# Kernel tuning notes

Hardware: AMD Instinct MI355X
Metric: run time of the kernel (lower is better)

The kernel has to match this reference:

```python
import jax, jax.numpy as jnp
import numpy as np

HID, INTER, DK = 768, 1536, 128
NEG_INF = 1.0e12
LOG512 = float(np.log(512.0))


def setup_inputs() -> dict:
    key = jax.random.key(0)
    k1, k2, k3 = jax.random.split(key, 3)
    B, S = 4, 2048
    hidden_states = jax.random.normal(k1, (B, S, HID), dtype=jnp.float32)
    attention_mask = jnp.ones((B, S), dtype=jnp.int32)
    # i_dense: hidden -> 2*INTER + DK (no bias); o_dense: INTER -> hidden (no bias)
    Wi = jax.random.normal(k2, (HID, 2 * INTER + DK), dtype=jnp.float32) * (HID ** -0.5)
    Wo = jax.random.normal(k3, (INTER, HID), dtype=jnp.float32) * (INTER ** -0.5)
    q_gamma = jnp.ones((DK,), dtype=jnp.float32)  # ScaleOffset scale, offset=False
    k_gamma = jnp.ones((DK,), dtype=jnp.float32)
    return {"hidden_states": hidden_states, "Wi": Wi, "Wo": Wo,
            "q_gamma": q_gamma, "k_gamma": k_gamma,
            "attention_mask": attention_mask}


def reference(hidden_states, Wi, Wo, q_gamma, k_gamma, attention_mask):
    # i_dense + swish, then split into u, v, qk
    x = jax.nn.silu(jnp.einsum('bsh,ho->bso', hidden_states, Wi))
    u = x[..., :INTER]
    v = x[..., INTER:2 * INTER]
    qk = x[..., 2 * INTER:]
    q = qk * q_gamma
    k = qk * k_gamma
    # single-head attention scores
    a = jnp.einsum('bmd,bnd->bmn', q, k) / (DK ** 0.5)
    mask = attention_mask[:, None, :]  # [B,1,N]
    a = jnp.where(mask == 0, -NEG_INF, a)
    l = jnp.sum(attention_mask, axis=-1, keepdims=True)[:, :, None].astype(a.dtype)  # [B,1,1]
    # softmax_plus: softmax(a * log(l) / log(512))
    A = jax.nn.softmax(a * jnp.log(l) / LOG512, axis=-1)
    # dropout inactive in eval mode
    o = jnp.einsum('bmi,ih->bmh', u * jnp.einsum('bmn,bnd->bmd', A, v), Wo)
    return o
```

## Files before the change

### kernel.cpp

```cpp
#include <hip/hip_runtime.h>
#include <hip/hip_bf16.h>
#include <math.h>

#define BATCH 4
#define SEQ   2048
#define HID   768
#define INTER 1536
#define DK    128
#define NTOT  3200
#define NTOTP 3328
#define MROWS 8192
#define LN512 6.2383246250395075f

typedef _Float16 half8   __attribute__((ext_vector_type(8)));
typedef _Float16 half4   __attribute__((ext_vector_type(4)));
typedef float    floatx4 __attribute__((ext_vector_type(4)));
typedef float    floatx16 __attribute__((ext_vector_type(16)));

typedef const __attribute__((address_space(1))) unsigned int* gas1_t;
typedef __attribute__((address_space(3))) unsigned int* las3_t;

static __device__ __forceinline__ void load16(const _Float16* g, _Float16* l) {
    __builtin_amdgcn_global_load_lds((gas1_t)g, (las3_t)l, 16, 0, 0);
}
#define WAIT_VM(N)    asm volatile("s_waitcnt vmcnt(" #N ")" ::: "memory")
#define WAIT_LGKM0()  asm volatile("s_waitcnt lgkmcnt(0)" ::: "memory")
#define BARRIER_RAW() asm volatile("s_barrier" ::: "memory")

__global__ void cast_h_kernel(const float* __restrict__ in, _Float16* __restrict__ out, int n) {
    int i = (blockIdx.x * blockDim.x + threadIdx.x) * 8;
    if (i < n) {
        float4 a = *reinterpret_cast<const float4*>(in + i);
        float4 b = *reinterpret_cast<const float4*>(in + i + 4);
        half8 h = {(_Float16)a.x, (_Float16)a.y, (_Float16)a.z, (_Float16)a.w,
                   (_Float16)b.x, (_Float16)b.y, (_Float16)b.z, (_Float16)b.w};
        *reinterpret_cast<half8*>(out + i) = h;
    }
}

__global__ void trans_wi_kernel(const float* __restrict__ Wi, _Float16* __restrict__ WiT) {
    __shared__ _Float16 tile[32][33];
    const int c0 = blockIdx.x * 32, r0 = blockIdx.y * 32;
    const int tx = threadIdx.x, ty = threadIdx.y;
#pragma unroll
    for (int j = 0; j < 32; j += 8)
        tile[tx][ty + j] = (c0 + tx < NTOT)
            ? (_Float16)Wi[(size_t)(r0 + ty + j) * NTOT + c0 + tx]
            : (_Float16)0.0f;
    __syncthreads();
#pragma unroll
    for (int j = 0; j < 32; j += 8)
        WiT[(size_t)(c0 + ty + j) * HID + r0 + tx] = tile[ty + j][tx];
}

__global__ void trans_wo_kernel(const float* __restrict__ Wo, _Float16* __restrict__ WoT) {
    __shared__ _Float16 tile[32][33];
    const int c0 = blockIdx.x * 32, r0 = blockIdx.y * 32;
    const int tx = threadIdx.x, ty = threadIdx.y;
#pragma unroll
    for (int j = 0; j < 32; j += 8)
        tile[tx][ty + j] = (_Float16)Wo[(size_t)(r0 + ty + j) * HID + c0 + tx];
    __syncthreads();
#pragma unroll
    for (int j = 0; j < 32; j += 8)
        WoT[(size_t)(c0 + ty + j) * INTER + r0 + tx] = tile[ty + j][tx];
}

__global__ void mask_scales_kernel(const int* __restrict__ mask, float* __restrict__ scales) {
    __shared__ int sh[256];
    int b = blockIdx.x;
    int s = 0;
    for (int i = threadIdx.x; i < SEQ; i += 256) s += mask[b * SEQ + i];
    sh[threadIdx.x] = s;
    __syncthreads();
    for (int off = 128; off > 0; off >>= 1) {
        if (threadIdx.x < off) sh[threadIdx.x] += sh[threadIdx.x + off];
        __syncthreads();
    }
    if (threadIdx.x == 0) scales[b] = logf((float)sh[0]) / LN512;
}

struct TileCtx {
    int tid, wave, lane, quad, l16, l31, half, wm, wn, c0, c1;
};
static __device__ __forceinline__ TileCtx make_ctx() {
    TileCtx t;
    t.tid = threadIdx.x;
    t.wave = t.tid >> 6; t.lane = t.tid & 63;
    t.quad = t.lane >> 4; t.l16 = t.lane & 15;
    t.l31 = t.lane & 31;  t.half = t.lane >> 5;
    t.wm = (t.wave & 1) * 64;
    t.wn = (t.wave >> 1) * 64;
    t.c0 = t.tid;
    t.c1 = t.tid + 256;
    return t;
}

static __device__ __forceinline__ void gemm_mainloop_3s32(
    const TileCtx& t,
    const _Float16* __restrict__ Ag, int lda,
    const _Float16* __restrict__ Bg, int ldb,
    int K, _Float16* smem, floatx16 acc[2][2])
{
    const int r0i = t.c0 >> 2, s0 = (((r0i >> 1) ^ (r0i >> 3)) & 3);
    const int r1i = t.c1 >> 2, s1 = (((r1i >> 1) ^ (r1i >> 3)) & 3);
    const int ak0 = ((t.c0 & 3) ^ s0) * 8;
    const int ak1 = ((t.c1 & 3) ^ s1) * 8;
    const _Float16* a0 = Ag + (size_t)r0i * lda + ak0;
    const _Float16* a1 = Ag + (size_t)r1i * lda + ak1;
    const _Float16* b0 = Bg + (size_t)r0i * ldb + ak0;
    const _Float16* b1 = Bg + (size_t)r1i * ldb + ak1;
    _Float16* Asl = smem + t.c0 * 8;
    _Float16* Bsl = smem + 12288 + t.c0 * 8;
    const int nIter = K >> 5;

    const int fsw = ((t.l31 >> 1) ^ (t.l31 >> 3)) & 3;

    load16(a0, Asl);        load16(a1, Asl + 2048);
    load16(b0, Bsl);        load16(b1, Bsl + 2048);
    if (nIter > 1) {
        load16(a0 + 32, Asl + 4096); load16(a1 + 32, Asl + 6144);
        load16(b0 + 32, Bsl + 4096); load16(b1 + 32, Bsl + 6144);
    }

    int sc = 0, sp = 2;
    for (int k = 0; k < nIter; ++k) {
        if (k + 1 < nIter) { WAIT_VM(4); } else { WAIT_VM(0); }
        BARRIER_RAW();
        if (k + 2 < nIter) {
            const int off = sp * 4096;
            const int k0 = (k + 2) << 5;
            load16(a0 + k0, Asl + off); load16(a1 + k0, Asl + off + 2048);
            load16(b0 + k0, Bsl + off); load16(b1 + k0, Bsl + off + 2048);
        }
        const _Float16* Ab = smem + sc * 4096;
        const _Float16* Bb = smem + 12288 + sc * 4096;
        half8 af[2][2], bf[2][2];
#pragma unroll
        for (int mt = 0; mt < 2; ++mt)
#pragma unroll
            for (int h = 0; h < 2; ++h)
                af[mt][h] = *reinterpret_cast<const half8*>(
                    Ab + (t.wm + mt * 32 + t.l31) * 32 + (((h * 2 + t.half) ^ fsw) * 8));
#pragma unroll
        for (int nt = 0; nt < 2; ++nt)
#pragma unroll
            for (int h = 0; h < 2; ++h)
                bf[nt][h] = *reinterpret_cast<const half8*>(
                    Bb + (t.wn + nt * 32 + t.l31) * 32 + (((h * 2 + t.half) ^ fsw) * 8));
#pragma unroll
        for (int h = 0; h < 2; ++h)
#pragma unroll
            for (int mt = 0; mt < 2; ++mt)
#pragma unroll
                for (int nt = 0; nt < 2; ++nt)
                    acc[mt][nt] = __builtin_amdgcn_mfma_f32_32x32x16_f16(af[mt][h], bf[nt][h], acc[mt][nt], 0, 0, 0);
        WAIT_LGKM0();
        sc = (sc == 2) ? 0 : sc + 1;
        sp = (sp == 2) ? 0 : sp + 1;
    }
}

__global__ __launch_bounds__(512, 2) void gemm1_kernel(
    const _Float16* __restrict__ Hb, const _Float16* __restrict__ WiT,
    const float* __restrict__ qg, const float* __restrict__ kg,
    _Float16* __restrict__ u, _Float16* __restrict__ vT,
    _Float16* __restrict__ q, _Float16* __restrict__ k)
{
    __shared__ _Float16 smem[65536];
    const int tid = threadIdx.x;
    const int lane = tid & 63, wave = tid >> 6;
    const int quad = lane >> 4, l16 = lane & 15;
    const int wm = wave >> 2, wn = wave & 3;

    const int f = blockIdx.x;
    const int xcd = f & 7, i = f >> 3;
    const int m0 = (xcd * 4 + (i & 3)) * 256;
    const int ntile = i >> 2;
    const int n0 = ntile * 256;

    const _Float16* Ag = Hb  + (size_t)m0 * HID;
    const _Float16* Bg = WiT + (size_t)n0 * HID;

    const int rA = tid >> 2;
    const int csw = ((tid & 3) ^ ((rA >> 1) & 3)) * 8;
    const _Float16* pa0 = Ag + (size_t)rA * HID + csw;
    const _Float16* pa1 = pa0 + (size_t)128 * HID;
    const _Float16* pb0 = Bg + (size_t)rA * HID + csw;
    const _Float16* pb1 = pb0 + (size_t)128 * HID;

    const int sw8 = (l16 >> 1) & 3;
    const int qs  = (quad ^ sw8) * 8;
    const int aoff = (wm * 128 + l16) * 32 + qs;
    const int boff = 8192 + (wn * 64 + l16) * 32 + qs;

    floatx4 acc[8][4] = {};

    const int nKt = HID / 32;

#pragma unroll
    for (int pt = 0; pt < 3; ++pt) {
        _Float16* ld = smem + pt * 16384 + tid * 8;
        const int ko = pt * 32;
        load16(pa0 + ko, ld);
        load16(pa1 + ko, ld + 4096);
        load16(pb0 + ko, ld + 8192);
        load16(pb1 + ko, ld + 12288);
    }
    WAIT_VM(8);
    BARRIER_RAW();

    for (int t = 0; t < nKt; ++t) {
        const _Float16* sl = smem + (t & 3) * 16384;
        if (t + 3 < nKt) {
            _Float16* ld = smem + ((t + 3) & 3) * 16384 + tid * 8;
            const int ko = (t + 3) * 32;
            load16(pa0 + ko, ld);        load16(pa1 + ko, ld + 4096);
            load16(pb0 + ko, ld + 8192); load16(pb1 + ko, ld + 12288);
        }
        half8 af[8], bf[4];
#pragma unroll
        for (int mt = 0; mt < 8; ++mt)
            af[mt] = *reinterpret_cast<const half8*>(sl + aoff + mt * 512);
#pragma unroll
        for (int nt = 0; nt < 4; ++nt)
            bf[nt] = *reinterpret_cast<const half8*>(sl + boff + nt * 512);
        __builtin_amdgcn_s_setprio(1);
#pragma unroll
        for (int mt = 0; mt < 8; ++mt)
#pragma unroll
            for (int nt = 0; nt < 4; ++nt)
                acc[mt][nt] = __builtin_amdgcn_mfma_f32_16x16x32_f16(af[mt], bf[nt], acc[mt][nt], 0, 0, 0);
        __builtin_amdgcn_s_setprio(0);
        if (t <= nKt - 4)      { WAIT_VM(8); }
        else if (t == nKt - 3) { WAIT_VM(4); }
        else if (t == nKt - 2) { WAIT_VM(0); }
        BARRIER_RAW();
    }
    __syncthreads();

    if (ntile < 6) {
#pragma unroll
        for (int mt = 0; mt < 8; ++mt) {
#pragma unroll
            for (int nt = 0; nt < 4; ++nt) {
                const int col = n0 + wn * 64 + nt * 16 + l16;
#pragma unroll
                for (int i2 = 0; i2 < 4; ++i2) {
                    const int row = m0 + wm * 128 + mt * 16 + quad * 4 + i2;
                    float x = acc[mt][nt][i2];
                    float y = x / (1.0f + __expf(-x));
                    u[(size_t)row * INTER + col] = (_Float16)y;
                }
            }
        }
    } else if (ntile < 12) {
        const int bb = m0 >> 11, sloc = m0 & (SEQ - 1), cI = n0 - INTER;
#pragma unroll
        for (int mt = 0; mt < 8; ++mt) {
#pragma unroll
            for (int nt = 0; nt < 4; ++nt) {
                const int cl  = wn * 64 + nt * 16 + l16;
                const int rl0 = wm * 128 + mt * 16 + quad * 4;
                half4 pk;
#pragma unroll
                for (int i2 = 0; i2 < 4; ++i2) {
                    float x = acc[mt][nt][i2];
                    pk[i2] = (_Float16)(x / (1.0f + __expf(-x)));
                }
                *reinterpret_cast<half4*>(smem + cl * 256 + (rl0 ^ ((cl & 31) << 3))) = pk;
            }
        }
        __syncthreads();
#pragma unroll
        for (int p = 0; p < 16; ++p) {
            const int chunk = p * 512 + tid;
            const int cl = chunk >> 5, scn = chunk & 31;
            half8 v = *reinterpret_cast<const half8*>(smem + cl * 256 + ((scn ^ (cl & 31)) << 3));
            *reinterpret_cast<half8*>(vT + ((size_t)bb * INTER + cI + cl) * SEQ + sloc + scn * 8) = v;
        }
    } else {
        if (wn < 2) {
#pragma unroll
            for (int mt = 0; mt < 8; ++mt) {
#pragma unroll
                for (int nt = 0; nt < 4; ++nt) {
                    const int cq = wn * 64 + nt * 16 + l16;
                    const float qgv = qg[cq], kgv = kg[cq];
#pragma unroll
                    for (int i2 = 0; i2 < 4; ++i2) {
                        const int row = m0 + wm * 128 + mt * 16 + quad * 4 + i2;
                        float x = acc[mt][nt][i2];
                        float y = x / (1.0f + __expf(-x));
                        q[(size_t)row * DK + cq] = (_Float16)(y * qgv);
                        k[(size_t)row * DK + cq] = (_Float16)(y * kgv);
                    }
                }
            }
        }
    }
}

__global__ __launch_bounds__(256) void scores_kernel(
    const _Float16* __restrict__ q, const _Float16* __restrict__ k,
    const int* __restrict__ mask, const float* __restrict__ scales,
    _Float16* __restrict__ P)
{
    const int f = blockIdx.x;
    const int xcd = f & 7, i = f >> 3;
    const int b = xcd >> 1;
    const int m0 = ((xcd & 1) * 64 + i) * 16;
    const int tid = threadIdx.x;
    const int wave = tid >> 6, lane = tid & 63, quad = lane >> 4, l16 = lane & 15;
    const float scale = scales[b];

    half8 aq[4];
    const _Float16* qrow = q + (b * SEQ + m0 + l16) * DK + quad * 8;
#pragma unroll
    for (int kk = 0; kk < 4; ++kk) aq[kk] = *reinterpret_cast<const half8*>(qrow + kk * 32);

    floatx4 sc[32];
#pragma unroll
    for (int nt = 0; nt < 32; ++nt) {
        int n0 = nt * 64 + wave * 16;
        const _Float16* krow = k + (b * SEQ + n0 + l16) * DK + quad * 8;
        floatx4 acc = {};
#pragma unroll
        for (int kk = 0; kk < 4; ++kk) {
            half8 bq = *reinterpret_cast<const half8*>(krow + kk * 32);
            acc = __builtin_amdgcn_mfma_f32_16x16x32_f16(aq[kk], bq, acc, 0, 0, 0);
        }
        sc[nt] = acc;
    }

    const float rs = 0.08838834764831845f * scale;
    const float mval = -1e12f * scale;
    float rmax[4] = {-3.4e38f, -3.4e38f, -3.4e38f, -3.4e38f};
#pragma unroll
    for (int nt = 0; nt < 32; ++nt) {
        int ncol = nt * 64 + wave * 16 + l16;
        bool mok = mask[b * SEQ + ncol] != 0;
#pragma unroll
        for (int i2 = 0; i2 < 4; ++i2) {
            float s = mok ? sc[nt][i2] * rs : mval;
            sc[nt][i2] = s;
            rmax[i2] = fmaxf(rmax[i2], s);
        }
    }
#pragma unroll
    for (int i2 = 0; i2 < 4; ++i2) {
#pragma unroll
        for (int off = 1; off < 16; off <<= 1)
            rmax[i2] = fmaxf(rmax[i2], __shfl_xor(rmax[i2], off, 64));
    }
    __shared__ float redmax[4][16];
    __shared__ float redsum[4][16];
    if (l16 == 0) {
#pragma unroll
        for (int i2 = 0; i2 < 4; ++i2) redmax[wave][quad * 4 + i2] = rmax[i2];
    }
    __syncthreads();
#pragma unroll
    for (int i2 = 0; i2 < 4; ++i2) {
        int r = quad * 4 + i2;
        rmax[i2] = fmaxf(fmaxf(redmax[0][r], redmax[1][r]), fmaxf(redmax[2][r], redmax[3][r]));
    }
    float rsum[4] = {0.f, 0.f, 0.f, 0.f};
#pragma unroll
    for (int nt = 0; nt < 32; ++nt) {
#pragma unroll
        for (int i2 = 0; i2 < 4; ++i2) {
            float e = __expf(sc[nt][i2] - rmax[i2]);
            sc[nt][i2] = e;
            rsum[i2] += e;
        }
    }
#pragma unroll
    for (int i2 = 0; i2 < 4; ++i2) {
#pragma unroll
        for (int off = 1; off < 16; off <<= 1) rsum[i2] += __shfl_xor(rsum[i2], off, 64);
    }
    if (l16 == 0) {
#pragma unroll
        for (int i2 = 0; i2 < 4; ++i2) redsum[wave][quad * 4 + i2] = rsum[i2];
    }
    __syncthreads();
#pragma unroll
    for (int i2 = 0; i2 < 4; ++i2) {
        int r = quad * 4 + i2;
        float tot = redsum[0][r] + redsum[1][r] + redsum[2][r] + redsum[3][r];
        float inv = 1.0f / tot;
        int row = m0 + r;
        _Float16* Prow = P + ((size_t)b * SEQ + row) * SEQ;
#pragma unroll
        for (int nt = 0; nt < 32; ++nt) {
            int ncol = nt * 64 + wave * 16 + l16;
            Prow[ncol] = (_Float16)(sc[nt][i2] * inv);
        }
    }
}

__global__ __launch_bounds__(256) void pv_kernel(
    const _Float16* __restrict__ P, const _Float16* __restrict__ vT,
    _Float16* __restrict__ u)
{
    __shared__ _Float16 smem[24576];
    TileCtx t = make_ctx();
    const int f = blockIdx.x;
    const int xcd = f & 7, i = f >> 3;
    const int b = i / 24, j = i % 24;
    const int m0 = (xcd * 2 + (j & 1)) * 128;
    const int n0 = (j >> 1) * 128;
    const _Float16* Pb  = P  + (size_t)b * SEQ * SEQ;
    const _Float16* vTb = vT + (size_t)b * INTER * SEQ;

    floatx16 acc[2][2] = {};
    gemm_mainloop_3s32(t, Pb + (size_t)m0 * SEQ, SEQ, vTb + (size_t)n0 * SEQ, SEQ, SEQ, smem, acc);

#pragma unroll
    for (int mt = 0; mt < 2; ++mt) {
#pragma unroll
        for (int nt = 0; nt < 2; ++nt) {
            int col = n0 + t.wn + nt * 32 + t.l31;
#pragma unroll
            for (int reg = 0; reg < 16; ++reg) {
                int row = m0 + t.wm + mt * 32 + (reg & 3) + 8 * (reg >> 2) + 4 * t.half;
                size_t gidx = ((size_t)(b * SEQ + row)) * INTER + col;
                float uv = (float)u[gidx];
                u[gidx] = (_Float16)(acc[mt][nt][reg] * uv);
            }
        }
    }
}

__global__ __launch_bounds__(256) void gemm2_kernel(
    const _Float16* __restrict__ tin, const _Float16* __restrict__ WoT,
    float* __restrict__ out)
{
    __shared__ _Float16 smem[24576];
    TileCtx t = make_ctx();
    const int f = blockIdx.x;
    const int xcd = f & 7, i = f >> 3;
    const int m0 = ((xcd << 3) | (i & 7)) * 128;
    const int n0 = (i >> 3) * 128;

    floatx16 acc[2][2] = {};
    gemm_mainloop_3s32(t, tin + (size_t)m0 * INTER, INTER, WoT + (size_t)n0 * INTER, INTER, INTER, smem, acc);

#pragma unroll
    for (int mt = 0; mt < 2; ++mt) {
#pragma unroll
        for (int nt = 0; nt < 2; ++nt) {
            int col = n0 + t.wn + nt * 32 + t.l31;
#pragma unroll
            for (int reg = 0; reg < 16; ++reg) {
                int row = m0 + t.wm + mt * 32 + (reg & 3) + 8 * (reg >> 2) + 4 * t.half;
                out[(size_t)row * HID + col] = acc[mt][nt][reg];
            }
        }
    }
}

extern "C" void kernel_launch(void* const* d_in, const int* in_sizes, int n_in,
                              void* d_out, int out_size, void* d_ws, size_t ws_size,
                              hipStream_t stream) {
    const float* H    = (const float*)d_in[0];
    const float* Wi   = (const float*)d_in[1];
    const float* Wo   = (const float*)d_in[2];
    const float* qg   = (const float*)d_in[3];
    const float* kg   = (const float*)d_in[4];
    const int*   mask = (const int*)d_in[5];
    float* out = (float*)d_out;

    char* base = (char*)d_ws;
    size_t off = 0;
    auto alloc = [&](size_t bytes) { void* p = base + off; off = (off + bytes + 255) & ~(size_t)255; return p; };
    _Float16* Hb   = (_Float16*)alloc((size_t)MROWS * HID * 2);
    _Float16* WiT  = (_Float16*)alloc((size_t)NTOTP * HID * 2);
    _Float16* WoT  = (_Float16*)alloc((size_t)HID * INTER * 2);
    _Float16* u    = (_Float16*)alloc((size_t)MROWS * INTER * 2);
    _Float16* vT   = (_Float16*)alloc((size_t)BATCH * INTER * SEQ * 2);
    _Float16* q    = (_Float16*)alloc((size_t)MROWS * DK * 2);
    _Float16* k    = (_Float16*)alloc((size_t)MROWS * DK * 2);
    _Float16* P    = (_Float16*)alloc((size_t)BATCH * SEQ * SEQ * 2);
    float*    scales = (float*)alloc(4 * sizeof(float));

    {
        int n = MROWS * HID;
        cast_h_kernel<<<n / 8 / 256, 256, 0, stream>>>(H, Hb, n);
        trans_wi_kernel<<<dim3(NTOTP / 32, HID / 32), dim3(32, 8), 0, stream>>>(Wi, WiT);
        trans_wo_kernel<<<dim3(HID / 32, INTER / 32), dim3(32, 8), 0, stream>>>(Wo, WoT);
        mask_scales_kernel<<<BATCH, 256, 0, stream>>>(mask, scales);
    }
    gemm1_kernel<<<416, 512, 0, stream>>>(Hb, WiT, qg, kg, u, vT, q, k);
    scores_kernel<<<512, 256, 0, stream>>>(q, k, mask, scales, P);
    pv_kernel<<<768, 256, 0, stream>>>(P, vT, u);
    gemm2_kernel<<<384, 256, 0, stream>>>(u, WoT, out);
}
```

Baseline: 304.5 us.

## Rework shared GEMM mainloop with 4-stage column-major LDS pipeline and priority hints

Replaces the 3-stage swizzled LDS mainloop used by the PV and output GEMMs with a 4-buffer pipeline that prefetches three K-tiles ahead, stores tiles in a k-chunk-major layout instead of an XOR swizzle, and moves the barrier to the end of each iteration. It also raises wave priority around the MFMA block. The aim is to hide more global-load latency and drop the per-iteration LDS wait. The cost is more shared memory per block (32K halves), which may lower occupancy, and the new layout may bring LDS bank conflicts back.

```diff
diff --git a/kernel.cpp b/kernel.cpp
--- a/kernel.cpp
+++ b/kernel.cpp
@@ -24,7 +24,6 @@
     __builtin_amdgcn_global_load_lds((gas1_t)g, (las3_t)l, 16, 0, 0);
 }
 #define WAIT_VM(N)    asm volatile("s_waitcnt vmcnt(" #N ")" ::: "memory")
-#define WAIT_LGKM0()  asm volatile("s_waitcnt lgkmcnt(0)" ::: "memory")
 #define BARRIER_RAW() asm volatile("s_barrier" ::: "memory")
 
 __global__ void cast_h_kernel(const float* __restrict__ in, _Float16* __restrict__ out, int n) {
@@ -81,7 +80,7 @@
 }
 
 struct TileCtx {
-    int tid, wave, lane, quad, l16, l31, half, wm, wn, c0, c1;
+    int tid, wave, lane, quad, l16, l31, half, wm, wn;
 };
 static __device__ __forceinline__ TileCtx make_ctx() {
     TileCtx t;
@@ -91,63 +90,61 @@
     t.l31 = t.lane & 31;  t.half = t.lane >> 5;
     t.wm = (t.wave & 1) * 64;
     t.wn = (t.wave >> 1) * 64;
-    t.c0 = t.tid;
-    t.c1 = t.tid + 256;
     return t;
 }
 
-static __device__ __forceinline__ void gemm_mainloop_3s32(
+static __device__ __forceinline__ void gemm_mainloop_cm32(
     const TileCtx& t,
     const _Float16* __restrict__ Ag, int lda,
     const _Float16* __restrict__ Bg, int ldb,
     int K, _Float16* smem, floatx16 acc[2][2])
 {
-    const int r0i = t.c0 >> 2, s0 = (((r0i >> 1) ^ (r0i >> 3)) & 3);
-    const int r1i = t.c1 >> 2, s1 = (((r1i >> 1) ^ (r1i >> 3)) & 3);
-    const int ak0 = ((t.c0 & 3) ^ s0) * 8;
-    const int ak1 = ((t.c1 & 3) ^ s1) * 8;
-    const _Float16* a0 = Ag + (size_t)r0i * lda + ak0;
-    const _Float16* a1 = Ag + (size_t)r1i * lda + ak1;
-    const _Float16* b0 = Bg + (size_t)r0i * ldb + ak0;
-    const _Float16* b1 = Bg + (size_t)r1i * ldb + ak1;
-    _Float16* Asl = smem + t.c0 * 8;
-    _Float16* Bsl = smem + 12288 + t.c0 * 8;
-    const int nIter = K >> 5;
-
-    const int fsw = ((t.l31 >> 1) ^ (t.l31 >> 3)) & 3;
-
-    load16(a0, Asl);        load16(a1, Asl + 2048);
-    load16(b0, Bsl);        load16(b1, Bsl + 2048);
-    if (nIter > 1) {
-        load16(a0 + 32, Asl + 4096); load16(a1 + 32, Asl + 6144);
-        load16(b0 + 32, Bsl + 4096); load16(b1 + 32, Bsl + 6144);
-    }
-
-    int sc = 0, sp = 2;
-    for (int k = 0; k < nIter; ++k) {
-        if (k + 1 < nIter) { WAIT_VM(4); } else { WAIT_VM(0); }
-        BARRIER_RAW();
-        if (k + 2 < nIter) {
-            const int off = sp * 4096;
-            const int k0 = (k + 2) << 5;
-            load16(a0 + k0, Asl + off); load16(a1 + k0, Asl + off + 2048);
-            load16(b0 + k0, Bsl + off); load16(b1 + k0, Bsl + off + 2048);
-        }
-        const _Float16* Ab = smem + sc * 4096;
-        const _Float16* Bb = smem + 12288 + sc * 4096;
+    const int rst = t.tid & 127;
+    const int c08 = (t.tid >> 7) * 8;
+    const _Float16* pa = Ag + (size_t)rst * lda + c08;
+    const _Float16* pb = Bg + (size_t)rst * ldb + c08;
+    const int nKt = K >> 5;
+
+    const int arow = t.wm + t.l31;
+    const int brow = t.wn + t.l31;
+
+#pragma unroll
+    for (int pt = 0; pt < 3; ++pt) {
+        _Float16* ld = smem + pt * 8192 + t.tid * 8;
+        const int ko = pt * 32;
+        load16(pa + ko,      ld);
+        load16(pa + ko + 16, ld + 2048);
+        load16(pb + ko,      ld + 4096);
+        load16(pb + ko + 16, ld + 6144);
+    }
+    WAIT_VM(8);
+    BARRIER_RAW();
+
+    for (int k = 0; k < nKt; ++k) {
+        const _Float16* Ab = smem + (k & 3) * 8192;
+        const _Float16* Bb = Ab + 4096;
+        if (k + 3 < nKt) {
+            _Float16* ld = smem + ((k + 3) & 3) * 8192 + t.tid * 8;
+            const int ko = (k + 3) * 32;
+            load16(pa + ko,      ld);
+            load16(pa + ko + 16, ld + 2048);
+            load16(pb + ko,      ld + 4096);
+            load16(pb + ko + 16, ld + 6144);
+        }
         half8 af[2][2], bf[2][2];
 #pragma unroll
         for (int mt = 0; mt < 2; ++mt)
 #pragma unroll
             for (int h = 0; h < 2; ++h)
                 af[mt][h] = *reinterpret_cast<const half8*>(
-                    Ab + (t.wm + mt * 32 + t.l31) * 32 + (((h * 2 + t.half) ^ fsw) * 8));
+                    Ab + (h * 2 + t.half) * 1024 + (arow + mt * 32) * 8);
 #pragma unroll
         for (int nt = 0; nt < 2; ++nt)
 #pragma unroll
             for (int h = 0; h < 2; ++h)
                 bf[nt][h] = *reinterpret_cast<const half8*>(
-                    Bb + (t.wn + nt * 32 + t.l31) * 32 + (((h * 2 + t.half) ^ fsw) * 8));
+                    Bb + (h * 2 + t.half) * 1024 + (brow + nt * 32) * 8);
+        __builtin_amdgcn_s_setprio(1);
 #pragma unroll
         for (int h = 0; h < 2; ++h)
 #pragma unroll
@@ -155,9 +152,11 @@
 #pragma unroll
                 for (int nt = 0; nt < 2; ++nt)
                     acc[mt][nt] = __builtin_amdgcn_mfma_f32_32x32x16_f16(af[mt][h], bf[nt][h], acc[mt][nt], 0, 0, 0);
-        WAIT_LGKM0();
-        sc = (sc == 2) ? 0 : sc + 1;
-        sp = (sp == 2) ? 0 : sp + 1;
+        __builtin_amdgcn_s_setprio(0);
+        if (k <= nKt - 4)      { WAIT_VM(8); }
+        else if (k == nKt - 3) { WAIT_VM(4); }
+        else if (k == nKt - 2) { WAIT_VM(0); }
+        BARRIER_RAW();
     }
 }
 
@@ -404,7 +403,7 @@
     const _Float16* __restrict__ P, const _Float16* __restrict__ vT,
     _Float16* __restrict__ u)
 {
-    __shared__ _Float16 smem[24576];
+    __shared__ _Float16 smem[32768];
     TileCtx t = make_ctx();
     const int f = blockIdx.x;
     const int xcd = f & 7, i = f >> 3;
@@ -415,7 +414,7 @@
     const _Float16* vTb = vT + (size_t)b * INTER * SEQ;
 
     floatx16 acc[2][2] = {};
-    gemm_mainloop_3s32(t, Pb + (size_t)m0 * SEQ, SEQ, vTb + (size_t)n0 * SEQ, SEQ, SEQ, smem, acc);
+    gemm_mainloop_cm32(t, Pb + (size_t)m0 * SEQ, SEQ, vTb + (size_t)n0 * SEQ, SEQ, SEQ, smem, acc);
 
 #pragma unroll
     for (int mt = 0; mt < 2; ++mt) {
@@ -437,7 +436,7 @@
     const _Float16* __restrict__ tin, const _Float16* __restrict__ WoT,
     float* __restrict__ out)
 {
-    __shared__ _Float16 smem[24576];
+    __shared__ _Float16 smem[32768];
     TileCtx t = make_ctx();
     const int f = blockIdx.x;
     const int xcd = f & 7, i = f >> 3;
@@ -445,7 +444,7 @@
     const int n0 = (i >> 3) * 128;
 
     floatx16 acc[2][2] = {};
-    gemm_mainloop_3s32(t, tin + (size_t)m0 * INTER, INTER, WoT + (size_t)n0 * INTER, INTER, INTER, smem, acc);
+    gemm_mainloop_cm32(t, tin + (size_t)m0 * INTER, INTER, WoT + (size_t)n0 * INTER, INTER, INTER, smem, acc);
 
 #pragma unroll
     for (int mt = 0; mt < 2; ++mt) {
```

Result: slower. 358.6 us (+17.8%).

## Merge prep kernels into one launch and stage P stores through LDS

Applied to the files above, without the earlier changes.

The four preprocessing kernels (cast H, transpose Wi, transpose Wo, mask scales) become one kernel that dispatches on block index, removing three launches and the gaps between them. The scores kernel now writes the normalized probabilities into a padded shared-memory tile and then copies whole rows to global memory with 16-byte vector stores, instead of scattered 2-byte stores. This adds about 64KB of LDS per block, which may lower occupancy in the scores kernel.

```diff
diff --git a/kernel.cpp b/kernel.cpp
--- a/kernel.cpp
+++ b/kernel.cpp
@@ -27,57 +27,58 @@
 #define WAIT_LGKM0()  asm volatile("s_waitcnt lgkmcnt(0)" ::: "memory")
 #define BARRIER_RAW() asm volatile("s_barrier" ::: "memory")
 
-__global__ void cast_h_kernel(const float* __restrict__ in, _Float16* __restrict__ out, int n) {
-    int i = (blockIdx.x * blockDim.x + threadIdx.x) * 8;
-    if (i < n) {
-        float4 a = *reinterpret_cast<const float4*>(in + i);
-        float4 b = *reinterpret_cast<const float4*>(in + i + 4);
+__global__ __launch_bounds__(256) void prep_kernel(
+    const float* __restrict__ H, _Float16* __restrict__ Hb,
+    const float* __restrict__ Wi, _Float16* __restrict__ WiT,
+    const float* __restrict__ Wo, _Float16* __restrict__ WoT,
+    const int* __restrict__ mask, float* __restrict__ scales)
+{
+    __shared__ _Float16 tile[32][33];
+    __shared__ int sh[256];
+    const int bid = blockIdx.x, tid = threadIdx.x;
+    if (bid < 3072) {
+        const int i = (bid * 256 + tid) * 8;
+        float4 a = *reinterpret_cast<const float4*>(H + i);
+        float4 b = *reinterpret_cast<const float4*>(H + i + 4);
         half8 h = {(_Float16)a.x, (_Float16)a.y, (_Float16)a.z, (_Float16)a.w,
                    (_Float16)b.x, (_Float16)b.y, (_Float16)b.z, (_Float16)b.w};
-        *reinterpret_cast<half8*>(out + i) = h;
-    }
-}
-
-__global__ void trans_wi_kernel(const float* __restrict__ Wi, _Float16* __restrict__ WiT) {
-    __shared__ _Float16 tile[32][33];
-    const int c0 = blockIdx.x * 32, r0 = blockIdx.y * 32;
-    const int tx = threadIdx.x, ty = threadIdx.y;
-#pragma unroll
-    for (int j = 0; j < 32; j += 8)
-        tile[tx][ty + j] = (c0 + tx < NTOT)
-            ? (_Float16)Wi[(size_t)(r0 + ty + j) * NTOT + c0 + tx]
-            : (_Float16)0.0f;
-    __syncthreads();
-#pragma unroll
-    for (int j = 0; j < 32; j += 8)
-        WiT[(size_t)(c0 + ty + j) * HID + r0 + tx] = tile[ty + j][tx];
-}
-
-__global__ void trans_wo_kernel(const float* __restrict__ Wo, _Float16* __restrict__ WoT) {
-    __shared__ _Float16 tile[32][33];
-    const int c0 = blockIdx.x * 32, r0 = blockIdx.y * 32;
-    const int tx = threadIdx.x, ty = threadIdx.y;
-#pragma unroll
-    for (int j = 0; j < 32; j += 8)
-        tile[tx][ty + j] = (_Float16)Wo[(size_t)(r0 + ty + j) * HID + c0 + tx];
-    __syncthreads();
-#pragma unroll
-    for (int j = 0; j < 32; j += 8)
-        WoT[(size_t)(c0 + ty + j) * INTER + r0 + tx] = tile[ty + j][tx];
-}
-
-__global__ void mask_scales_kernel(const int* __restrict__ mask, float* __restrict__ scales) {
-    __shared__ int sh[256];
-    int b = blockIdx.x;
-    int s = 0;
-    for (int i = threadIdx.x; i < SEQ; i += 256) s += mask[b * SEQ + i];
-    sh[threadIdx.x] = s;
-    __syncthreads();
-    for (int off = 128; off > 0; off >>= 1) {
-        if (threadIdx.x < off) sh[threadIdx.x] += sh[threadIdx.x + off];
+        *reinterpret_cast<half8*>(Hb + i) = h;
+    } else if (bid < 3072 + 2496) {
+        const int l = bid - 3072;
+        const int c0 = (l % 104) * 32, r0 = (l / 104) * 32;
+        const int tx = tid & 31, ty = tid >> 5;
+#pragma unroll
+        for (int j = 0; j < 32; j += 8)
+            tile[tx][ty + j] = (c0 + tx < NTOT)
+                ? (_Float16)Wi[(size_t)(r0 + ty + j) * NTOT + c0 + tx]
+                : (_Float16)0.0f;
         __syncthreads();
-    }
-    if (threadIdx.x == 0) scales[b] = logf((float)sh[0]) / LN512;
+#pragma unroll
+        for (int j = 0; j < 32; j += 8)
+            WiT[(size_t)(c0 + ty + j) * HID + r0 + tx] = tile[ty + j][tx];
+    } else if (bid < 3072 + 2496 + 1152) {
+        const int l = bid - (3072 + 2496);
+        const int c0 = (l % 24) * 32, r0 = (l / 24) * 32;
+        const int tx = tid & 31, ty = tid >> 5;
+#pragma unroll
+        for (int j = 0; j < 32; j += 8)
+            tile[tx][ty + j] = (_Float16)Wo[(size_t)(r0 + ty + j) * HID + c0 + tx];
+        __syncthreads();
+#pragma unroll
+        for (int j = 0; j < 32; j += 8)
+            WoT[(size_t)(c0 + ty + j) * INTER + r0 + tx] = tile[ty + j][tx];
+    } else {
+        const int b = bid - (3072 + 2496 + 1152);
+        int s = 0;
+        for (int i = tid; i < SEQ; i += 256) s += mask[b * SEQ + i];
+        sh[tid] = s;
+        __syncthreads();
+        for (int off = 128; off > 0; off >>= 1) {
+            if (tid < off) sh[tid] += sh[tid + off];
+            __syncthreads();
+        }
+        if (tid == 0) scales[b] = logf((float)sh[0]) / LN512;
+    }
 }
 
 struct TileCtx {
@@ -306,6 +307,9 @@
     const int* __restrict__ mask, const float* __restrict__ scales,
     _Float16* __restrict__ P)
 {
+    __shared__ _Float16 ps[16 * 2056];
+    __shared__ float redmax[4][16];
+    __shared__ float redsum[4][16];
     const int f = blockIdx.x;
     const int xcd = f & 7, i = f >> 3;
     const int b = xcd >> 1;
@@ -353,8 +357,6 @@
         for (int off = 1; off < 16; off <<= 1)
             rmax[i2] = fmaxf(rmax[i2], __shfl_xor(rmax[i2], off, 64));
     }
-    __shared__ float redmax[4][16];
-    __shared__ float redsum[4][16];
     if (l16 == 0) {
 #pragma unroll
         for (int i2 = 0; i2 < 4; ++i2) redmax[wave][quad * 4 + i2] = rmax[i2];
@@ -390,13 +392,20 @@
         int r = quad * 4 + i2;
         float tot = redsum[0][r] + redsum[1][r] + redsum[2][r] + redsum[3][r];
         float inv = 1.0f / tot;
-        int row = m0 + r;
-        _Float16* Prow = P + ((size_t)b * SEQ + row) * SEQ;
 #pragma unroll
         for (int nt = 0; nt < 32; ++nt) {
             int ncol = nt * 64 + wave * 16 + l16;
-            Prow[ncol] = (_Float16)(sc[nt][i2] * inv);
-        }
+            ps[r * 2056 + ncol] = (_Float16)(sc[nt][i2] * inv);
+        }
+    }
+    __syncthreads();
+    _Float16* Pb = P + ((size_t)b * SEQ + m0) * SEQ;
+#pragma unroll
+    for (int p = 0; p < 16; ++p) {
+        const int chunk = p * 256 + tid;
+        const int row = chunk >> 8, c8 = chunk & 255;
+        half8 v = *reinterpret_cast<const half8*>(ps + row * 2056 + c8 * 8);
+        *reinterpret_cast<half8*>(Pb + (size_t)row * SEQ + c8 * 8) = v;
     }
 }
 
@@ -485,13 +494,7 @@
     _Float16* P    = (_Float16*)alloc((size_t)BATCH * SEQ * SEQ * 2);
     float*    scales = (float*)alloc(4 * sizeof(float));
 
-    {
-        int n = MROWS * HID;
-        cast_h_kernel<<<n / 8 / 256, 256, 0, stream>>>(H, Hb, n);
-        trans_wi_kernel<<<dim3(NTOTP / 32, HID / 32), dim3(32, 8), 0, stream>>>(Wi, WiT);
-        trans_wo_kernel<<<dim3(HID / 32, INTER / 32), dim3(32, 8), 0, stream>>>(Wo, WoT);
-        mask_scales_kernel<<<BATCH, 256, 0, stream>>>(mask, scales);
-    }
+    prep_kernel<<<6724, 256, 0, stream>>>(H, Hb, Wi, WiT, Wo, WoT, mask, scales);
     gemm1_kernel<<<416, 512, 0, stream>>>(Hb, WiT, qg, kg, u, vT, q, k);
     scores_kernel<<<512, 256, 0, stream>>>(q, k, mask, scales, P);
     pv_kernel<<<768, 256, 0, stream>>>(P, vT, u);
```

New measurement: 296.5 us. 1.03x faster.
